# Performance work log

Hardware: AMD Instinct MI355X
Metric: run time of the kernel (lower is better)

Reference implementation:

```python
import jax, jax.numpy as jnp
import numpy as np

B, S, D, DH, H, NCLS, VOCAB, L = 16, 512, 512, 512, 8, 10000, 32000, 6
HD = DH // H  # 64


def _norm(X, gamma, beta, axis):
    # torch.var is unbiased by default -> ddof=1
    mu = jnp.mean(X, axis=axis, keepdims=True)
    var = jnp.var(X, axis=axis, ddof=1, keepdims=True)
    return gamma * ((X - mu) / jnp.sqrt(var + 1e-8)) + beta


def _pos_table(s, d):
    pos = np.arange(s, dtype=np.float64)[:, None]
    i = np.arange(d, dtype=np.float64)[None, :]
    angle = pos / np.power(10000.0, (i - (i % 2)) / d)
    tab = np.where((np.arange(d)[None, :] % 2) == 0, np.sin(angle), np.cos(angle))
    return jnp.asarray(tab, dtype=jnp.float32)


def _encoder(x, p):
    b, s, d = x.shape

    def heads(w):
        y = x @ w.T                         # [B,S,DH]
        y = y.reshape(b, s, HD, H)          # interleaved split: channel c -> head c%8
        return jnp.transpose(y, (3, 0, 1, 2))  # [H,B,S,HD]

    q, k, v = heads(p['WQ']), heads(p['WK']), heads(p['WV'])
    # scaling uses d_k = x.shape[-1] = hidden_dim (not head_dim), as in source
    e = jnp.einsum('hbsd,hbtd->hbst', q, k) / jnp.sqrt(jnp.float32(d))
    e = _norm(e, p['ga'].reshape(H, 1, 1, 1), p['ba'].reshape(H, 1, 1, 1), axis=3)
    alpha = jax.nn.softmax(e, axis=3)
    head = jnp.einsum('hbst,hbtd->hbsd', alpha, v)      # [H,B,S,HD]
    a = jnp.transpose(head, (1, 2, 0, 3)).reshape(b, s, DH)  # cat(head[0..7], dim=2)
    attn = a @ p['WO']                                   # [B,S,D]
    x2 = _norm(attn + x, p['g1'], p['b1n'], axis=2)
    ff = jax.nn.relu(x2 @ p['W1'] + p['b1']) @ p['W2'] + p['b2']
    return _norm(ff + x2, p['g2'], p['b2n'], axis=2)


def setup_inputs() -> dict:
    key = jax.random.key(0)
    ks = jax.random.split(key, 16)
    sc = 0.05  # scale randn params for numerical stability across 6 layers
    return {
        'x': jax.random.randint(ks[0], (B, S), 0, VOCAB),
        'embedded_matrix': jax.random.normal(ks[1], (VOCAB, D), jnp.float32) * sc,
        'WQ': jax.random.normal(ks[2], (L, DH, D), jnp.float32) * sc,
        'WK': jax.random.normal(ks[3], (L, DH, D), jnp.float32) * sc,
        'WV': jax.random.normal(ks[4], (L, DH, D), jnp.float32) * sc,
        'WO': jax.random.normal(ks[5], (L, DH, D), jnp.float32) * sc,
        'W1': jax.random.normal(ks[6], (L, D, 4 * D), jnp.float32) * sc,
        'b1': jax.random.normal(ks[7], (L, 4 * D), jnp.float32) * sc,
        'W2': jax.random.normal(ks[8], (L, 4 * D, D), jnp.float32) * sc,
        'b2': jax.random.normal(ks[9], (L, D), jnp.float32) * sc,
        'gamma_a': jnp.ones((L, H, 1), jnp.float32),
        'beta_a': jnp.zeros((L, H, 1), jnp.float32),
        'gamma1': jnp.ones((L,), jnp.float32),
        'beta1': jnp.zeros((L,), jnp.float32),
        'gamma2': jnp.ones((L,), jnp.float32),
        'beta2': jnp.zeros((L,), jnp.float32),
        'V_e': jax.random.normal(ks[10], (D, 1), jnp.float32) * sc,
        'V_d': jax.random.normal(ks[11], (S, NCLS), jnp.float32) * sc,
        'gamma_f': jnp.ones((), jnp.float32),
        'beta_f': jnp.zeros((), jnp.float32),
    }


def reference(x, embedded_matrix, WQ, WK, WV, WO, W1, b1, W2, b2,
              gamma_a, beta_a, gamma1, beta1, gamma2, beta2,
              V_e, V_d, gamma_f, beta_f):
    x1 = embedded_matrix[x]                 # [B,S,D]
    x2 = x1 + _pos_table(S, D)
    acc = x1 + x2                           # input to encoder1 = x2 + x1
    params = {'WQ': WQ, 'WK': WK, 'WV': WV, 'WO': WO,
              'W1': W1, 'b1': b1, 'W2': W2, 'b2': b2,
              'ga': gamma_a, 'ba': beta_a,
              'g1': gamma1, 'b1n': beta1, 'g2': gamma2, 'b2n': beta2}

    def step(carry, p):
        out = _encoder(carry, p)
        # dense residual: next input = sum of ALL previous layer outputs + x1 + x2
        return carry + out, out

    _, outs = jax.lax.scan(step, acc, params)
    x8 = outs[-1]                           # [B,S,D]
    x9 = x8 @ V_e                           # [B,S,1]
    z = jnp.swapaxes(x9, 1, 2) @ V_d        # [B,1,NCLS]
    z = _norm(z, gamma_f, beta_f, axis=2)
    return jax.nn.softmax(z, axis=2).reshape(B, NCLS)
```

## Files before the change

### kernel.cpp

```cpp
#include <hip/hip_runtime.h>
#include <hip/hip_bf16.h>
#include <math.h>

#define N_TOK 8192
#define DMODEL 512
#define NHEAD 8
#define HDIM 64
#define SEQ 512
#define BATCH 16
#define FFDIM 2048
#define NLAYER 6
#define NCLS 10000
#define VD_SC 8

typedef unsigned short u16;
typedef __attribute__((ext_vector_type(8))) short bf16x8;
typedef __attribute__((ext_vector_type(8))) unsigned short u16x8;
typedef __attribute__((ext_vector_type(4))) unsigned short u16x4;
typedef __attribute__((ext_vector_type(4))) float f32x4;

__device__ __forceinline__ u16 f2b(float x) {
    unsigned int u = __float_as_uint(x);
    u += 0x7fffu + ((u >> 16) & 1u);
    return (u16)(u >> 16);
}

__device__ __forceinline__ void gl_lds16(const void* g, void* l) {
    __builtin_amdgcn_global_load_lds(
        (const __attribute__((address_space(1))) unsigned int*)g,
        (__attribute__((address_space(3))) unsigned int*)l, 16, 0, 0);
}

__global__ __launch_bounds__(512) void pos_kernel(float* __restrict__ pos) {
    const int i = threadIdx.x;
    const int s0 = blockIdx.x * 32;
    const double bse = pow(10000.0, -(double)(i & ~1) / 512.0);
    const double cb = cos(bse), sb = sin(bse);
    const double a0 = (double)s0 * bse;
    double sn = sin(a0), cs = cos(a0);
    const bool odd = i & 1;
    for (int k = 0; k < 32; ++k) {
        pos[(size_t)(s0 + k) * 512 + i] = (float)(odd ? cs : sn);
        const double ns = sn * cb + cs * sb;
        cs = cs * cb - sn * sb;
        sn = ns;
    }
}

__global__ __launch_bounds__(256) void embed_kernel(const int* __restrict__ xi,
        const float* __restrict__ emb, const float* __restrict__ pos,
        float* __restrict__ C, u16* __restrict__ Cb) {
    const int idx = blockIdx.x * 256 + threadIdx.x;
    const int n = idx >> 7, d4 = (idx & 127) << 2;
    const int row = xi[n];
    const int s = n & 511;
    const float4 e = *(const float4*)&emb[(size_t)row * 512 + d4];
    const float4 p = *(const float4*)&pos[(size_t)s * 512 + d4];
    float4 o;
    o.x = 2.f * e.x + p.x; o.y = 2.f * e.y + p.y;
    o.z = 2.f * e.z + p.z; o.w = 2.f * e.w + p.w;
    *(float4*)&C[(size_t)n * 512 + d4] = o;
    u16x4 ob = { f2b(o.x), f2b(o.y), f2b(o.z), f2b(o.w) };
    *(u16x4*)&Cb[(size_t)n * 512 + d4] = ob;
}

__global__ __launch_bounds__(256) void cvt3_kernel(const float* __restrict__ q,
        const float* __restrict__ k, const float* __restrict__ v,
        u16* __restrict__ dst) {
    const int i = blockIdx.x * 256 + threadIdx.x;
    const int l = i / 196608;
    const int rem = i - l * 196608;
    const int m = rem >> 16, r = rem & 65535;
    const int j = r >> 7, col4 = r & 127;
    const int srow = (m == 2) ? j : ((j >> 6) | ((j & 63) << 3));
    const float* src = (m == 0 ? q : (m == 1 ? k : v));
    const float4 vv = ((const float4*)src)[(size_t)l * 65536 + srow * 128 + col4];
    u16x4 o = { f2b(vv.x), f2b(vv.y), f2b(vv.z), f2b(vv.w) };
    *(u16x4*)&dst[(size_t)l * 786432 + (size_t)m * 262144 + (size_t)(j * 128 + col4) * 4] = o;
}

__global__ __launch_bounds__(256) void tcvt_b16_kernel(const float* __restrict__ src,
        u16* __restrict__ dst, int Kd, int Nd) {
    __shared__ u16 t[64][65];
    const int k0 = blockIdx.x * 64, n0 = blockIdx.y * 64;
    const size_t off = (size_t)blockIdx.z * Kd * Nd;
    src += off; dst += off;
    const int cx = threadIdx.x & 63, r0 = threadIdx.x >> 6;
    #pragma unroll
    for (int i = 0; i < 16; ++i) {
        const int r = r0 * 16 + i;
        t[cx][r] = f2b(src[(size_t)(k0 + r) * Nd + n0 + cx]);
    }
    __syncthreads();
    #pragma unroll
    for (int i = 0; i < 16; ++i) {
        const int nn = r0 * 16 + i;
        dst[(size_t)(n0 + nn) * Kd + k0 + cx] = t[nn][cx];
    }
}

enum { EG_QKV3 = 0, EG_F32 = 1, EG_BIAS_F32 = 2, EG_BRELU_B16 = 3 };

template<int BM, int EPI>
__global__ __launch_bounds__(256)
void gemm_bf16(const u16* __restrict__ A, const u16* __restrict__ Bt,
               const float* __restrict__ bias, void* __restrict__ Cout,
               int N, int K) {
    constexpr int MF = BM / 32;
    __shared__ u16 As[2][BM * 64];
    __shared__ u16 Bs[2][128 * 64];
    const int tid = threadIdx.x, w = tid >> 6, l = tid & 63;
    const int g = l >> 4, c = l & 15;
    const int wm = w >> 1, wn = w & 1;
    const int bm = blockIdx.x * BM, bn = blockIdx.y * 128;
    const int sr = l >> 3, sc8 = l & 7;

    const f32x4 zero = {0.f, 0.f, 0.f, 0.f};
    f32x4 acc[MF][4];
    #pragma unroll
    for (int i = 0; i < MF; ++i)
        #pragma unroll
        for (int j = 0; j < 4; ++j) acc[i][j] = zero;

    auto stage = [&](int buf, int k0) {
        #pragma unroll
        for (int i = 0; i < MF; ++i) {
            const int rb = w * (BM / 4) + i * 8;
            const int r = rb + sr;
            const int ck = (sc8 ^ (r & 7)) * 8;
            gl_lds16(A + (size_t)(bm + r) * K + k0 + ck, &As[buf][rb * 64]);
        }
        #pragma unroll
        for (int i = 0; i < 4; ++i) {
            const int rb = w * 32 + i * 8;
            const int r = rb + sr;
            const int ck = (sc8 ^ (r & 7)) * 8;
            gl_lds16(Bt + (size_t)(bn + r) * K + k0 + ck, &Bs[buf][rb * 64]);
        }
    };

    auto compute = [&](int buf) {
        const char* Ab = (const char*)&As[buf][0];
        const char* Bb = (const char*)&Bs[buf][0];
        #pragma unroll
        for (int ks = 0; ks < 2; ++ks) {
            bf16x8 af[MF], bfv[4];
            #pragma unroll
            for (int q = 0; q < MF; ++q) {
                const int ra = wm * (BM / 2) + q * 16 + c;
                af[q] = *(const bf16x8*)(Ab +
                        ((ra * 128 + ks * 64 + g * 16) ^ ((ra & 7) << 4)));
            }
            #pragma unroll
            for (int q = 0; q < 4; ++q) {
                const int rb2 = wn * 64 + q * 16 + c;
                bfv[q] = *(const bf16x8*)(Bb +
                        ((rb2 * 128 + ks * 64 + g * 16) ^ ((rb2 & 7) << 4)));
            }
            #pragma unroll
            for (int mf = 0; mf < MF; ++mf)
                #pragma unroll
                for (int nf = 0; nf < 4; ++nf)
                    acc[mf][nf] = __builtin_amdgcn_mfma_f32_16x16x32_bf16(
                        af[mf], bfv[nf], acc[mf][nf], 0, 0, 0);
        }
    };

    stage(0, 0);
    int cur = 0;
    for (int k0 = 0; k0 + 64 < K; k0 += 64) {
        stage(cur ^ 1, k0 + 64);
        __builtin_amdgcn_sched_barrier(0);
        if (MF == 4) asm volatile("s_waitcnt vmcnt(8)" ::: "memory");
        else         asm volatile("s_waitcnt vmcnt(6)" ::: "memory");
        __builtin_amdgcn_s_barrier();
        __builtin_amdgcn_sched_barrier(0);
        compute(cur);
        __builtin_amdgcn_sched_barrier(0);
        __builtin_amdgcn_s_barrier();
        cur ^= 1;
    }
    asm volatile("s_waitcnt vmcnt(0)" ::: "memory");
    __builtin_amdgcn_s_barrier();
    __builtin_amdgcn_sched_barrier(0);
    compute(cur);

    #pragma unroll
    for (int mf = 0; mf < MF; ++mf) {
        #pragma unroll
        for (int nf = 0; nf < 4; ++nf) {
            const int n  = bn + wn * 64 + nf * 16 + c;
            const int m0 = bm + wm * (BM / 2) + mf * 16 + g * 4;
            if (EPI == EG_QKV3) {
                u16* o = (u16*)Cout;
                const int seg = n >> 9, nn = n & 511;
                if (seg < 2) {
                    u16* dst = o + (size_t)seg * 4194304;
                    #pragma unroll
                    for (int r = 0; r < 4; ++r)
                        dst[(size_t)(m0 + r) * 512 + nn] = f2b(acc[mf][nf][r]);
                } else {
                    u16* dst = o + (size_t)2 * 4194304;
                    const int h = nn & 7, d = nn >> 3, bb = m0 >> 9, s0 = m0 & 511;
                    u16x4 pk = { f2b(acc[mf][nf][0]), f2b(acc[mf][nf][1]),
                                 f2b(acc[mf][nf][2]), f2b(acc[mf][nf][3]) };
                    *(u16x4*)&dst[((size_t)(h * 16 + bb) * 64 + d) * 512 + s0] = pk;
                }
            } else if (EPI == EG_F32) {
                float* o = (float*)Cout;
                #pragma unroll
                for (int r = 0; r < 4; ++r)
                    o[(size_t)(m0 + r) * N + n] = acc[mf][nf][r];
            } else if (EPI == EG_BIAS_F32) {
                float* o = (float*)Cout;
                const float bv = bias[n];
                #pragma unroll
                for (int r = 0; r < 4; ++r)
                    o[(size_t)(m0 + r) * N + n] = acc[mf][nf][r] + bv;
            } else {
                u16* o = (u16*)Cout;
                const float bv = bias[n];
                #pragma unroll
                for (int r = 0; r < 4; ++r)
                    o[(size_t)(m0 + r) * N + n] = f2b(fmaxf(acc[mf][nf][r] + bv, 0.f));
            }
        }
    }
}

__global__ __launch_bounds__(256, 2)
void attn_mfma(const u16* __restrict__ Qb, const u16* __restrict__ Kb,
               const u16* __restrict__ Vt, const float* __restrict__ ga,
               const float* __restrict__ ba, u16* __restrict__ A, float scale) {
    __shared__ __align__(16) u16 KV[2][8192];
    __shared__ __align__(16) u16 P[4][2][16][136];
    const int bid = blockIdx.x;
    const int hb = bid & 127, qc = bid >> 7;
    const int h = hb >> 4, b = hb & 15;
    const int tid = threadIdx.x, w = tid >> 6, l = tid & 63;
    const int g = l >> 4, c = l & 15;
    const float gah = ga[h], bah = ba[h];
    const size_t tok0 = (size_t)b * SEQ;
    const int hoff = h * 64;
    const size_t vtbase = ((size_t)(h * 16 + b)) * 64 * 512;
    const int q0 = qc * 64 + w * 16;
    const int swz = (c & 7) << 4;
    const int srK = l >> 3, scK = l & 7;
    const int srV = l >> 4, scV = l & 15;

    #pragma unroll
    for (int i = 0; i < 4; ++i) {
        const int rb = w * 32 + i * 8;
        const int r = rb + srK;
        gl_lds16(Kb + (tok0 + r) * 512 + hoff + (scK ^ (r & 7)) * 8,
                 &KV[0][rb * 64]);
    }
    const u16* qrow = Qb + (tok0 + q0 + c) * 512 + hoff;
    const bf16x8 qf0 = *(const bf16x8*)(qrow + g * 8);
    const bf16x8 qf1 = *(const bf16x8*)(qrow + 32 + g * 8);
    __syncthreads();

    f32x4 acc[32];
    int buf = 0;
    #pragma unroll
    for (int ch = 0; ch < 4; ++ch) {
        if (ch < 3) {
            #pragma unroll
            for (int i = 0; i < 4; ++i) {
                const int rb = w * 32 + i * 8;
                const int r = rb + srK;
                gl_lds16(Kb + (tok0 + (ch + 1) * 128 + r) * 512 + hoff + (scK ^ (r & 7)) * 8,
                         &KV[buf ^ 1][rb * 64]);
            }
        }
        const char* kb = (const char*)&KV[buf][0];
        #pragma unroll
        for (int tt = 0; tt < 8; ++tt) {
            const int r = tt * 16 + c;
            const int sx = (r & 7) << 4;
            const char* rowp = kb + r * 128;
            const bf16x8 kf0 = *(const bf16x8*)(rowp + ((g * 16) ^ sx));
            const bf16x8 kf1 = *(const bf16x8*)(rowp + ((64 + g * 16) ^ sx));
            f32x4 z = {0.f, 0.f, 0.f, 0.f};
            z = __builtin_amdgcn_mfma_f32_16x16x32_bf16(kf0, qf0, z, 0, 0, 0);
            z = __builtin_amdgcn_mfma_f32_16x16x32_bf16(kf1, qf1, z, 0, 0, 0);
            acc[ch * 8 + tt] = z;
        }
        if (ch < 3) { __syncthreads(); buf ^= 1; }
    }

    #pragma unroll
    for (int i = 0; i < 4; ++i) {
        const int db = w * 16 + i * 4;
        const int d = db + srV;
        gl_lds16(Vt + vtbase + (size_t)d * 512 + (scV ^ (d & 7)) * 8,
                 &KV[0][db * 128]);
    }

    float sm = 0.f, sq = 0.f;
    #pragma unroll
    for (int t = 0; t < 32; ++t)
        #pragma unroll
        for (int r = 0; r < 4; ++r) {
            const float v = acc[t][r];
            sm += v; sq = fmaf(v, v, sq);
        }
    sm += __shfl_xor(sm, 16); sm += __shfl_xor(sm, 32);
    sq += __shfl_xor(sq, 16); sq += __shfl_xor(sq, 32);

    const float LOG2E = 1.4426950408889634f;
    const float S  = sm * scale;
    const float Qq = sq * scale * scale;
    const float mu = S * (1.f / 512.f);
    const float var = (Qq - 512.f * mu * mu) * (1.f / 511.f);
    const float rg = rsqrtf(var + 1e-8f) * gah;
    const float A2 = scale * rg * LOG2E;
    const float B2 = (bah - mu * rg) * LOG2E;

    __syncthreads();

    float se = 0.f;
    f32x4 oacc[4];
    #pragma unroll
    for (int dt = 0; dt < 4; ++dt) oacc[dt] = (f32x4){0.f, 0.f, 0.f, 0.f};

    int vbuf = 0;
    #pragma unroll
    for (int ch = 0; ch < 4; ++ch) {
        if (ch < 3) {
            #pragma unroll
            for (int i = 0; i < 4; ++i) {
                const int db = w * 16 + i * 4;
                const int d = db + srV;
                gl_lds16(Vt + vtbase + (size_t)d * 512 + (ch + 1) * 128 + (scV ^ (d & 7)) * 8,
                         &KV[vbuf ^ 1][db * 128]);
            }
        }
        char* pbase = (char*)&P[w][ch & 1][0][0];
        #pragma unroll
        for (int tt = 0; tt < 8; ++tt) {
            const int t = ch * 8 + tt;
            float p0 = exp2f(fmaf(acc[t][0], A2, B2));
            float p1 = exp2f(fmaf(acc[t][1], A2, B2));
            float p2 = exp2f(fmaf(acc[t][2], A2, B2));
            float p3 = exp2f(fmaf(acc[t][3], A2, B2));
            se += (p0 + p1) + (p2 + p3);
            u16x4 pk = { f2b(p0), f2b(p1), f2b(p2), f2b(p3) };
            *(u16x4*)(pbase + c * 272 + ((tt * 32 + g * 8) ^ swz)) = pk;
        }
        const char* vb = (const char*)&KV[vbuf][0];
        #pragma unroll
        for (int ks = 0; ks < 4; ++ks) {
            const bf16x8 pf = *(const bf16x8*)(pbase + c * 272 + ((ks * 64 + g * 16) ^ swz));
            #pragma unroll
            for (int dt = 0; dt < 4; ++dt) {
                const int d = dt * 16 + c;
                const bf16x8 vf = *(const bf16x8*)(vb + d * 256 +
                        ((ks * 64 + g * 16) ^ ((d & 7) << 4)));
                oacc[dt] = __builtin_amdgcn_mfma_f32_16x16x32_bf16(pf, vf, oacc[dt], 0, 0, 0);
            }
        }
        if (ch < 3) { __syncthreads(); vbuf ^= 1; }
    }

    se += __shfl_xor(se, 16); se += __shfl_xor(se, 32);
    const float inv = 1.f / se;
    float iv[4];
    #pragma unroll
    for (int r = 0; r < 4; ++r) iv[r] = __shfl(inv, g * 4 + r);
    #pragma unroll
    for (int dt = 0; dt < 4; ++dt)
        #pragma unroll
        for (int r = 0; r < 4; ++r)
            A[((size_t)(b * 512 + q0 + g * 4 + r)) * 512 + h * 64 + dt * 16 + c] =
                f2b(oacc[dt][r] * iv[r]);
}

__global__ __launch_bounds__(256)
void ln_res_kernel(const float* __restrict__ X, const float* __restrict__ R,
                   const float* __restrict__ gp, const float* __restrict__ bp,
                   int lidx, float* __restrict__ Y, u16* __restrict__ Yb,
                   float* __restrict__ Cacc, u16* __restrict__ Cb) {
    const int tid = threadIdx.x, w = tid >> 6, l = tid & 63;
    const size_t row = (size_t)blockIdx.x * 4 + w;
    const float g = gp[lidx], bb = bp[lidx];
    const float* x = X + row * 512;
    const float* r = R + row * 512;
    float v[8];
    const float4 a0 = *(const float4*)&x[l * 8], a1 = *(const float4*)&x[l * 8 + 4];
    const float4 r0 = *(const float4*)&r[l * 8], r1 = *(const float4*)&r[l * 8 + 4];
    v[0] = a0.x + r0.x; v[1] = a0.y + r0.y; v[2] = a0.z + r0.z; v[3] = a0.w + r0.w;
    v[4] = a1.x + r1.x; v[5] = a1.y + r1.y; v[6] = a1.z + r1.z; v[7] = a1.w + r1.w;
    float s = 0.f, sq = 0.f;
    #pragma unroll
    for (int i = 0; i < 8; ++i) { s += v[i]; sq = fmaf(v[i], v[i], sq); }
    #pragma unroll
    for (int o = 1; o < 64; o <<= 1) { s += __shfl_xor(s, o); sq += __shfl_xor(sq, o); }
    const float mu   = s * (1.f / 512.f);
    const float var  = (sq - 512.f * mu * mu) * (1.f / 511.f);
    const float rstd = rsqrtf(var + 1e-8f);
    float y[8];
    #pragma unroll
    for (int i = 0; i < 8; ++i) y[i] = fmaf((v[i] - mu) * rstd, g, bb);
    if (Y) {
        *(float4*)&Y[row * 512 + l * 8]     = *(float4*)&y[0];
        *(float4*)&Y[row * 512 + l * 8 + 4] = *(float4*)&y[4];
    }
    if (Yb) {
        u16x8 yb;
        #pragma unroll
        for (int i = 0; i < 8; ++i) yb[i] = f2b(y[i]);
        *(u16x8*)&Yb[row * 512 + l * 8] = yb;
    }
    if (Cacc) {
        float cv[8];
        float4 c0 = *(float4*)&Cacc[row * 512 + l * 8];
        float4 c1 = *(float4*)&Cacc[row * 512 + l * 8 + 4];
        cv[0] = c0.x + y[0]; cv[1] = c0.y + y[1]; cv[2] = c0.z + y[2]; cv[3] = c0.w + y[3];
        cv[4] = c1.x + y[4]; cv[5] = c1.y + y[5]; cv[6] = c1.z + y[6]; cv[7] = c1.w + y[7];
        *(float4*)&Cacc[row * 512 + l * 8]     = *(float4*)&cv[0];
        *(float4*)&Cacc[row * 512 + l * 8 + 4] = *(float4*)&cv[4];
        u16x8 cb;
        #pragma unroll
        for (int i = 0; i < 8; ++i) cb[i] = f2b(cv[i]);
        *(u16x8*)&Cb[row * 512 + l * 8] = cb;
    }
}

__global__ __launch_bounds__(256)
void fin_ve_kernel(const float* __restrict__ X8, const float* __restrict__ Ve,
                   float* __restrict__ x9) {
    const int tid = threadIdx.x, w = tid >> 6, l = tid & 63;
    const size_t row = (size_t)blockIdx.x * 4 + w;
    const float* x = X8 + row * 512;
    float s = 0.f;
    #pragma unroll
    for (int i = 0; i < 8; ++i) s = fmaf(x[l * 8 + i], Ve[l * 8 + i], s);
    #pragma unroll
    for (int o = 1; o < 64; o <<= 1) s += __shfl_xor(s, o);
    if (l == 0) x9[row] = s;
}

__global__ __launch_bounds__(256)
void fin_vd_part(const float* __restrict__ x9, const float* __restrict__ Vd,
                 float* __restrict__ zp) {
    __shared__ float xs[16][64];
    const int tid = threadIdx.x;
    const int c = blockIdx.x * 256 + tid;
    const int sc = blockIdx.y, s0 = sc * 64;
    #pragma unroll
    for (int p = 0; p < 4; ++p) {
        const int idx = p * 256 + tid;
        xs[idx >> 6][idx & 63] = x9[(idx >> 6) * 512 + s0 + (idx & 63)];
    }
    __syncthreads();
    float acc[16];
    #pragma unroll
    for (int b = 0; b < 16; ++b) acc[b] = 0.f;
    if (c < NCLS) {
        for (int s = 0; s < 64; ++s) {
            const float vd = Vd[(size_t)(s0 + s) * NCLS + c];
            #pragma unroll
            for (int b = 0; b < 16; ++b) acc[b] = fmaf(xs[b][s], vd, acc[b]);
        }
    }
    #pragma unroll
    for (int b = 0; b < 16; ++b)
        zp[((size_t)sc * 16 + b) * 10240 + c] = acc[b];
}

__global__ __launch_bounds__(256)
void fin_sm_kernel(const float* __restrict__ zp, const float* __restrict__ gp,
                   const float* __restrict__ bp, float* __restrict__ out) {
    __shared__ float zs[NCLS];
    __shared__ float red[4];
    __shared__ float red2[4];
    const int b = blockIdx.x, tid = threadIdx.x, w = tid >> 6, l = tid & 63;
    float s = 0.f, sq = 0.f;
    for (int i = tid; i < NCLS; i += 256) {
        float v = 0.f;
        #pragma unroll
        for (int sc = 0; sc < VD_SC; ++sc)
            v += zp[((size_t)sc * 16 + b) * 10240 + i];
        zs[i] = v; s += v; sq = fmaf(v, v, sq);
    }
    #pragma unroll
    for (int o = 1; o < 64; o <<= 1) { s += __shfl_xor(s, o); sq += __shfl_xor(sq, o); }
    if (l == 0) { red[w] = s; red2[w] = sq; }
    __syncthreads();
    s  = red[0] + red[1] + red[2] + red[3];
    sq = red2[0] + red2[1] + red2[2] + red2[3];
    const float mu   = s / 10000.f;
    const float var  = (sq - 10000.f * mu * mu) / 9999.f;
    const float rstd = rsqrtf(var + 1e-8f);
    const float g = gp[0], be = bp[0];
    __syncthreads();
    float mx = -1e30f;
    for (int i = tid; i < NCLS; i += 256) {
        const float e = fmaf((zs[i] - mu) * rstd, g, be);
        zs[i] = e; mx = fmaxf(mx, e);
    }
    #pragma unroll
    for (int o = 1; o < 64; o <<= 1) mx = fmaxf(mx, __shfl_xor(mx, o));
    if (l == 0) red[w] = mx;
    __syncthreads();
    mx = fmaxf(fmaxf(red[0], red[1]), fmaxf(red[2], red[3]));
    float es = 0.f;
    for (int i = tid; i < NCLS; i += 256) {
        const float p = expf(zs[i] - mx);
        zs[i] = p; es += p;
    }
    #pragma unroll
    for (int o = 1; o < 64; o <<= 1) es += __shfl_xor(es, o);
    if (l == 0) red2[w] = es;
    __syncthreads();
    es = red2[0] + red2[1] + red2[2] + red2[3];
    const float inv = 1.f / es;
    for (int i = tid; i < NCLS; i += 256) out[(size_t)b * NCLS + i] = zs[i] * inv;
}

extern "C" void kernel_launch(void* const* d_in, const int* in_sizes, int n_in,
                              void* d_out, int out_size, void* d_ws, size_t ws_size,
                              hipStream_t stream) {
    (void)in_sizes; (void)n_in; (void)out_size; (void)ws_size;
    const int*   xi  = (const int*)d_in[0];
    const float* emb = (const float*)d_in[1];
    const float* WQ  = (const float*)d_in[2];
    const float* WK  = (const float*)d_in[3];
    const float* WV  = (const float*)d_in[4];
    const float* WO  = (const float*)d_in[5];
    const float* W1  = (const float*)d_in[6];
    const float* b1  = (const float*)d_in[7];
    const float* W2  = (const float*)d_in[8];
    const float* b2  = (const float*)d_in[9];
    const float* ga  = (const float*)d_in[10];
    const float* ba  = (const float*)d_in[11];
    const float* g1  = (const float*)d_in[12];
    const float* be1 = (const float*)d_in[13];
    const float* g2  = (const float*)d_in[14];
    const float* be2 = (const float*)d_in[15];
    const float* Ve  = (const float*)d_in[16];
    const float* Vd  = (const float*)d_in[17];
    const float* gf  = (const float*)d_in[18];
    const float* bf  = (const float*)d_in[19];
    float* out = (float*)d_out;

    float* ws  = (float*)d_ws;
    float* pos = ws;
    float* C   = pos + 262144;
    float* X2  = C   + 4194304;
    float* OUT = X2  + 4194304;
    float* PF  = OUT + 4194304;
    u16* ub = (u16*)(PF + 4194304);
    u16* Cb  = ub;  ub += 4194304;
    u16* X2b = ub;  ub += 4194304;
    u16* Qbf = ub;  ub += 4194304;
    u16* Kbf = ub;  ub += 4194304;
    u16* Vtb = ub;  ub += 4194304;
    u16* Abf = ub;  ub += 4194304;
    u16* Hb  = Qbf;
    float* zp = (float*)Vtb;
    u16* WQKVb = ub; ub += 4718592;
    u16* WOt = ub; ub += 1572864;
    u16* W1t = ub; ub += 6291456;
    u16* W2t = ub; ub += 6291456;
    float* x9 = (float*)ub;

    pos_kernel<<<16, 512, 0, stream>>>(pos);
    embed_kernel<<<4096, 256, 0, stream>>>(xi, emb, pos, C, Cb);

    cvt3_kernel<<<4608, 256, 0, stream>>>(WQ, WK, WV, WQKVb);
    tcvt_b16_kernel<<<dim3(8,  8, 6), 256, 0, stream>>>(WO, WOt, 512, 512);
    tcvt_b16_kernel<<<dim3(8, 32, 6), 256, 0, stream>>>(W1, W1t, 512, 2048);
    tcvt_b16_kernel<<<dim3(32, 8, 6), 256, 0, stream>>>(W2, W2t, 2048, 512);

    const float scale = 1.0f / sqrtf(512.0f);

    for (int l = 0; l < NLAYER; ++l) {
        const u16* wqkv = WQKVb + (size_t)l * 786432;
        const u16* wo = WOt + (size_t)l * 262144;
        const u16* w1 = W1t + (size_t)l * 1048576;
        const u16* w2 = W2t + (size_t)l * 1048576;

        gemm_bf16<128, EG_QKV3>     <<<dim3(64, 12), 256, 0, stream>>>(Cb, wqkv, nullptr, Qbf, 1536, 512);
        attn_mfma                   <<<1024, 256, 0, stream>>>(Qbf, Kbf, Vtb, ga + l*8, ba + l*8, Abf, scale);
        gemm_bf16<64, EG_F32>       <<<dim3(128, 4), 256, 0, stream>>>(Abf, wo, nullptr, PF, 512, 512);
        ln_res_kernel               <<<2048, 256, 0, stream>>>(PF, C, g1, be1, l, X2, X2b, nullptr, nullptr);
        gemm_bf16<128, EG_BRELU_B16><<<dim3(64, 16), 256, 0, stream>>>(X2b, w1, b1 + l*2048, Hb, 2048, 512);
        gemm_bf16<64, EG_BIAS_F32>  <<<dim3(128, 4), 256, 0, stream>>>(Hb, w2, b2 + l*512, PF, 512, 2048);
        ln_res_kernel               <<<2048, 256, 0, stream>>>(PF, X2, g2, be2, l,
                                                               (l == NLAYER - 1) ? OUT : nullptr,
                                                               nullptr, C, Cb);
    }

    fin_ve_kernel<<<2048, 256, 0, stream>>>(OUT, Ve, x9);
    fin_vd_part<<<dim3(40, VD_SC), 256, 0, stream>>>(x9, Vd, zp);
    fin_sm_kernel<<<16, 256, 0, stream>>>(zp, gf, bf, out);
}
```

Before: 938.5 us.

## Switch GEMM to triple-buffered K=32 LDS pipeline with two-stage prefetch

The bf16 GEMM now stages K tiles of 32 instead of 64 into three LDS buffers, prefetching two tiles ahead rather than one. The swizzle and the per-lane staging layout are reworked for 64-byte rows, and the waitcnt thresholds are adjusted per stage. The aim is better overlap of global loads with MFMA work while keeping LDS usage about the same. In exchange, each barrier-bounded step has half the compute, so there are more barriers per K.

```diff
diff --git a/kernel.cpp b/kernel.cpp
--- a/kernel.cpp
+++ b/kernel.cpp
@@ -107,13 +107,14 @@
                const float* __restrict__ bias, void* __restrict__ Cout,
                int N, int K) {
     constexpr int MF = BM / 32;
-    __shared__ u16 As[2][BM * 64];
-    __shared__ u16 Bs[2][128 * 64];
+    constexpr int ASZ = BM * 32, BSZ = 128 * 32;
+    __shared__ u16 As[3][ASZ];
+    __shared__ u16 Bs[3][BSZ];
     const int tid = threadIdx.x, w = tid >> 6, l = tid & 63;
     const int g = l >> 4, c = l & 15;
     const int wm = w >> 1, wn = w & 1;
     const int bm = blockIdx.x * BM, bn = blockIdx.y * 128;
-    const int sr = l >> 3, sc8 = l & 7;
+    const int srow = l >> 2, sseg = l & 3;
 
     const f32x4 zero = {0.f, 0.f, 0.f, 0.f};
     f32x4 acc[MF][4];
@@ -122,68 +123,72 @@
         #pragma unroll
         for (int j = 0; j < 4; ++j) acc[i][j] = zero;
 
-    auto stage = [&](int buf, int k0) {
-        #pragma unroll
-        for (int i = 0; i < MF; ++i) {
-            const int rb = w * (BM / 4) + i * 8;
-            const int r = rb + sr;
-            const int ck = (sc8 ^ (r & 7)) * 8;
-            gl_lds16(A + (size_t)(bm + r) * K + k0 + ck, &As[buf][rb * 64]);
-        }
-        #pragma unroll
-        for (int i = 0; i < 4; ++i) {
-            const int rb = w * 32 + i * 8;
-            const int r = rb + sr;
-            const int ck = (sc8 ^ (r & 7)) * 8;
-            gl_lds16(Bt + (size_t)(bn + r) * K + k0 + ck, &Bs[buf][rb * 64]);
+    auto stage = [&](int buf, int kt) {
+        const int k0 = kt * 32;
+        #pragma unroll
+        for (int i = 0; i < BM / 64; ++i) {
+            const int rb = w * (BM / 4) + i * 16;
+            const int r = rb + srow;
+            gl_lds16(A + (size_t)(bm + r) * K + k0 + (sseg ^ (r & 3)) * 8,
+                     &As[buf][rb * 32]);
+        }
+        #pragma unroll
+        for (int i = 0; i < 2; ++i) {
+            const int rb = w * 32 + i * 16;
+            const int r = rb + srow;
+            gl_lds16(Bt + (size_t)(bn + r) * K + k0 + (sseg ^ (r & 3)) * 8,
+                     &Bs[buf][rb * 32]);
         }
     };
 
     auto compute = [&](int buf) {
         const char* Ab = (const char*)&As[buf][0];
         const char* Bb = (const char*)&Bs[buf][0];
-        #pragma unroll
-        for (int ks = 0; ks < 2; ++ks) {
-            bf16x8 af[MF], bfv[4];
+        bf16x8 af[MF], bfv[4];
+        #pragma unroll
+        for (int q = 0; q < MF; ++q) {
+            const int ra = wm * (BM / 2) + q * 16 + c;
+            af[q] = *(const bf16x8*)(Ab + ra * 64 + ((g * 16) ^ ((ra & 3) << 4)));
+        }
+        #pragma unroll
+        for (int q = 0; q < 4; ++q) {
+            const int rb2 = wn * 64 + q * 16 + c;
+            bfv[q] = *(const bf16x8*)(Bb + rb2 * 64 + ((g * 16) ^ ((rb2 & 3) << 4)));
+        }
+        #pragma unroll
+        for (int mf = 0; mf < MF; ++mf)
             #pragma unroll
-            for (int q = 0; q < MF; ++q) {
-                const int ra = wm * (BM / 2) + q * 16 + c;
-                af[q] = *(const bf16x8*)(Ab +
-                        ((ra * 128 + ks * 64 + g * 16) ^ ((ra & 7) << 4)));
-            }
-            #pragma unroll
-            for (int q = 0; q < 4; ++q) {
-                const int rb2 = wn * 64 + q * 16 + c;
-                bfv[q] = *(const bf16x8*)(Bb +
-                        ((rb2 * 128 + ks * 64 + g * 16) ^ ((rb2 & 7) << 4)));
-            }
-            #pragma unroll
-            for (int mf = 0; mf < MF; ++mf)
-                #pragma unroll
-                for (int nf = 0; nf < 4; ++nf)
-                    acc[mf][nf] = __builtin_amdgcn_mfma_f32_16x16x32_bf16(
-                        af[mf], bfv[nf], acc[mf][nf], 0, 0, 0);
-        }
+            for (int nf = 0; nf < 4; ++nf)
+                acc[mf][nf] = __builtin_amdgcn_mfma_f32_16x16x32_bf16(
+                    af[mf], bfv[nf], acc[mf][nf], 0, 0, 0);
     };
 
+    const int NS = K >> 5;
     stage(0, 0);
-    int cur = 0;
-    for (int k0 = 0; k0 + 64 < K; k0 += 64) {
-        stage(cur ^ 1, k0 + 64);
-        __builtin_amdgcn_sched_barrier(0);
-        if (MF == 4) asm volatile("s_waitcnt vmcnt(8)" ::: "memory");
-        else         asm volatile("s_waitcnt vmcnt(6)" ::: "memory");
+    stage(1, 1);
+    int buf = 0;
+    for (int s = 0; s < NS; ++s) {
+        if (s + 2 < NS) {
+            int nb = buf + 2; if (nb >= 3) nb -= 3;
+            stage(nb, s + 2);
+            __builtin_amdgcn_sched_barrier(0);
+            if (MF == 4) asm volatile("s_waitcnt vmcnt(8)" ::: "memory");
+            else         asm volatile("s_waitcnt vmcnt(6)" ::: "memory");
+        } else if (s + 1 < NS) {
+            __builtin_amdgcn_sched_barrier(0);
+            if (MF == 4) asm volatile("s_waitcnt vmcnt(4)" ::: "memory");
+            else         asm volatile("s_waitcnt vmcnt(3)" ::: "memory");
+        } else {
+            __builtin_amdgcn_sched_barrier(0);
+            asm volatile("s_waitcnt vmcnt(0)" ::: "memory");
+        }
         __builtin_amdgcn_s_barrier();
         __builtin_amdgcn_sched_barrier(0);
-        compute(cur);
+        compute(buf);
         __builtin_amdgcn_sched_barrier(0);
         __builtin_amdgcn_s_barrier();
-        cur ^= 1;
-    }
-    asm volatile("s_waitcnt vmcnt(0)" ::: "memory");
-    __builtin_amdgcn_s_barrier();
-    __builtin_amdgcn_sched_barrier(0);
-    compute(cur);
+        if (++buf == 3) buf = 0;
+    }
 
     #pragma unroll
     for (int mf = 0; mf < MF; ++mf) {
```

New measurement: 986.6 us. 1.05x slower.
